# Optimization experiments

Measured on AMD Instinct MI355X. Metric: run time of the kernel, lower is better.

Reference implementation:

```python
import math
import jax, jax.numpy as jnp
import numpy as np


def setup_inputs() -> dict:
    key = jax.random.key(0)
    k1, k2 = jax.random.split(key)
    b, t, h, d = 2, 2048, 16, 64
    q = jax.random.normal(k1, (b, t, h, d), dtype=jnp.float32)
    kv = jax.random.normal(k2, (b, t, 2, h, d), dtype=jnp.float32)
    return {"q": q, "kv": kv}


def reference(q, kv):
    # Padded cross-attention branch, causal=False, dropout=0 (identity).
    d = q.shape[-1]
    softmax_scale = 1.0 / math.sqrt(d)
    k = kv[:, :, 0]  # [b, s, h, d]
    v = kv[:, :, 1]  # [b, s, h, d]
    # scores: [b, h, t, s] -- full score matrix, matching torch einsum
    scores = jnp.einsum('bthd,bshd->bhts', q, k * softmax_scale)
    attention = jax.nn.softmax(scores, axis=-1)
    out = jnp.einsum('bhts,bshd->bthd', attention, v)
    return out
```

## Files before the change

kernel.cpp:

```cpp
#include <hip/hip_runtime.h>
#include <hip/hip_bf16.h>

typedef __attribute__((ext_vector_type(8))) short v8s;
typedef __attribute__((ext_vector_type(4))) float v4f;
typedef unsigned long long u64;
typedef unsigned short u16;

#define BB 2
#define TT 2048
#define HH 16
#define DD 64


__device__ __forceinline__ unsigned short f2bf(float f) {
    unsigned int u = __builtin_bit_cast(unsigned int, f);
    u = u + 0x7FFFu + ((u >> 16) & 1u);
    return (unsigned short)(u >> 16);
}

__device__ __forceinline__ unsigned cvt2(float a, float b) {
    return ((unsigned)f2bf(b) << 16) | (unsigned)f2bf(a);
}

__device__ __forceinline__ v8s cvt8s(const float4& lo, const float4& hi, float s) {
    union { v8s v; unsigned u[4]; } r;
    r.u[0] = cvt2(lo.x * s, lo.y * s);
    r.u[1] = cvt2(lo.z * s, lo.w * s);
    r.u[2] = cvt2(hi.x * s, hi.y * s);
    r.u[3] = cvt2(hi.z * s, hi.w * s);
    return r.v;
}

__device__ __forceinline__ unsigned cvtpk(float lo, float hi) {
    unsigned r;
    asm("v_cvt_pk_bf16_f32 %0, %1, %2" : "=v"(r) : "v"(lo), "v"(hi));
    return r;
}

__device__ __forceinline__ v8s pack8(u64 lo, u64 hi) {
    union { v8s v; u64 q[2]; } u;
    u.q[0] = lo; u.q[1] = hi;
    return u.v;
}

typedef __attribute__((address_space(1))) const unsigned int gas_u32;
typedef __attribute__((address_space(3))) unsigned int las_u32;
__device__ __forceinline__ void gl_lds16(const void* g, void* l) {
    __builtin_amdgcn_global_load_lds((gas_u32*)g, (las_u32*)l, 16, 0, 0);
}


__global__ __launch_bounds__(256)
void prep_kv(const float* __restrict__ kvg, u16* __restrict__ wsK, u16* __restrict__ wsV) {
    __shared__ u16 vlds[64][72];
    const int wg   = blockIdx.x;
    const int tile = wg & 31;
    const int h    = (wg >> 5) & 15;
    const int b    = wg >> 9;
    const int t    = threadIdx.x;
    const int s0   = tile * 64;

    u16* kout = wsK + (((size_t)(b * 16 + h) * 32 + tile) * 4096);
    u16* vout = wsV + (((size_t)(b * 16 + h) * 32 + tile) * 4096);

    #pragma unroll
    for (int i = 0; i < 2; ++i) {
        int id  = t + 256 * i;
        int row = id >> 3;
        int bi  = id & 7;
        int c   = bi >> 2, lg = bi & 3;
        const float* kp = kvg + ((((size_t)(b * TT + s0 + row) * 2 + 0) * HH + h) * DD + 32 * c + 4 * lg);
        float4 ka = *(const float4*)kp;
        float4 kb = *(const float4*)(kp + 16);
        *(v8s*)((char*)kout + row * 128 + ((bi ^ (row & 7)) << 4)) = cvt8s(ka, kb, 1.0f);
    }
    #pragma unroll
    for (int i = 0; i < 2; ++i) {
        int id  = t + 256 * i;
        int row = id >> 3;
        int d8  = id & 7;
        const float* vp = kvg + ((((size_t)(b * TT + s0 + row) * 2 + 1) * HH + h) * DD + 8 * d8);
        float4 va = *(const float4*)vp;
        float4 vb = *(const float4*)(vp + 4);
        *(v8s*)&vlds[row][8 * d8] = cvt8s(va, vb, 1.0f);
    }
    __syncthreads();
    #pragma unroll
    for (int i = 0; i < 2; ++i) {
        int id = t + 256 * i;
        int dd = id >> 3;
        int bi = id & 7;
        int ks = bi >> 2, lg = bi & 3;
        union { v8s v; u16 w[8]; } r;
        #pragma unroll
        for (int j = 0; j < 4; ++j) {
            r.w[j]     = vlds[32 * ks + 4 * lg + j][dd];
            r.w[4 + j] = vlds[32 * ks + 16 + 4 * lg + j][dd];
        }
        *(v8s*)((char*)vout + dd * 128 + ((bi ^ (dd & 7)) << 4)) = r.v;
    }
}


__global__ __launch_bounds__(512, 4)
void attn_v4(const float* __restrict__ qg, const u16* __restrict__ wsK,
             const u16* __restrict__ wsV, float* __restrict__ outg) {
    __shared__ __align__(16) u16 KT[2][4096];
    __shared__ __align__(16) u16 VT[2][4096];

    const int bid  = blockIdx.x;
    const int wgid = (bid & 7) * 64 + (bid >> 3);
    const int qt   = wgid & 15;
    const int h    = (wgid >> 4) & 15;
    const int b    = wgid >> 8;
    const int tid  = threadIdx.x;
    const int lane = tid & 63;
    const int wid  = tid >> 6;
    const int lr   = lane & 15;
    const int lg   = lane >> 4;

    const u16* kbase = wsK + (size_t)(b * 16 + h) * 131072;
    const u16* vbase = wsV + (size_t)(b * 16 + h) * 131072;

    const int q0 = qt * 128 + wid * 16;

    const float qscale = 0.125f * 1.4426950408889634f;
    v8s qf[2];
    {
        const float* qb = qg + ((size_t)((b * TT + q0 + lr) * HH + h)) * DD;
        #pragma unroll
        for (int c = 0; c < 2; ++c) {
            float4 lo = *(const float4*)(qb + 32 * c + 4 * lg);
            float4 hi = *(const float4*)(qb + 32 * c + 4 * lg + 16);
            qf[c] = cvt8s(lo, hi, qscale);
        }
    }

#define STAGE(buf, tt)                                                                        \
    do {                                                                                      \
        gl_lds16(kbase + (size_t)(tt) * 4096 + tid * 8, (char*)&KT[buf][0] + wid * 1024);     \
        gl_lds16(vbase + (size_t)(tt) * 4096 + tid * 8, (char*)&VT[buf][0] + wid * 1024);     \
    } while (0)

    STAGE(0, 0);

    v4f oa[4];
    #pragma unroll
    for (int dc = 0; dc < 4; ++dc)
        #pragma unroll
        for (int r = 0; r < 4; ++r) oa[dc][r] = 0.0f;
    float m = -INFINITY, lsum = 0.0f;

    for (int t = 0; t < 32; ++t) {
        const int cur = t & 1;
        if (t < 31) {
            STAGE(cur ^ 1, t + 1);
            asm volatile("s_waitcnt vmcnt(2)" ::: "memory");
        } else {
            asm volatile("s_waitcnt vmcnt(0)" ::: "memory");
        }
        __builtin_amdgcn_s_barrier();

        const char* kb = (const char*)&KT[cur][0];
        const char* vb = (const char*)&VT[cur][0];

        v4f st[4];
        #pragma unroll
        for (int rb = 0; rb < 4; ++rb)
            #pragma unroll
            for (int r = 0; r < 4; ++r) st[rb][r] = 0.0f;
        __builtin_amdgcn_s_setprio(1);
        #pragma unroll
        for (int c = 0; c < 2; ++c) {
            #pragma unroll
            for (int rb = 0; rb < 4; ++rb) {
                int s = 16 * rb + lr;
                v8s kf = *(const v8s*)(kb + s * 128 + (((4 * c + lg) ^ (s & 7)) << 4));
                st[rb] = __builtin_amdgcn_mfma_f32_16x16x32_bf16(kf, qf[c], st[rb], 0, 0, 0);
            }
        }
        __builtin_amdgcn_s_setprio(0);

        float mc = st[0][0];
        #pragma unroll
        for (int rb = 0; rb < 4; ++rb)
            #pragma unroll
            for (int r = 0; r < 4; ++r) mc = fmaxf(mc, st[rb][r]);
        mc = fmaxf(mc, __shfl_xor(mc, 16));
        mc = fmaxf(mc, __shfl_xor(mc, 32));
        if (!__all(mc - m <= 8.0f)) {
            float mnew  = fmaxf(m, mc);
            float alpha = __builtin_amdgcn_exp2f(m - mnew);
            lsum *= alpha;
            m = mnew;
            float a0 = __shfl(alpha, 4 * lg + 0);
            float a1 = __shfl(alpha, 4 * lg + 1);
            float a2 = __shfl(alpha, 4 * lg + 2);
            float a3 = __shfl(alpha, 4 * lg + 3);
            #pragma unroll
            for (int dc = 0; dc < 4; ++dc) {
                oa[dc][0] *= a0; oa[dc][1] *= a1;
                oa[dc][2] *= a2; oa[dc][3] *= a3;
            }
        }
        float ps = 0.0f;
        #pragma unroll
        for (int rb = 0; rb < 4; ++rb)
            #pragma unroll
            for (int r = 0; r < 4; ++r) {
                float e = __builtin_amdgcn_exp2f(st[rb][r] - m);
                st[rb][r] = e;
                ps += e;
            }
        ps += __shfl_xor(ps, 16);
        ps += __shfl_xor(ps, 32);
        lsum += ps;

        v8s pf[2];
        #pragma unroll
        for (int ks = 0; ks < 2; ++ks) {
            union { v8s v; unsigned u[4]; } r;
            r.u[0] = cvtpk(st[2 * ks][0],     st[2 * ks][1]);
            r.u[1] = cvtpk(st[2 * ks][2],     st[2 * ks][3]);
            r.u[2] = cvtpk(st[2 * ks + 1][0], st[2 * ks + 1][1]);
            r.u[3] = cvtpk(st[2 * ks + 1][2], st[2 * ks + 1][3]);
            pf[ks] = r.v;
        }

        __builtin_amdgcn_s_setprio(1);
        #pragma unroll
        for (int ks = 0; ks < 2; ++ks) {
            #pragma unroll
            for (int dc = 0; dc < 4; ++dc) {
                int d = 16 * dc + lr;
                v8s vf = *(const v8s*)(vb + d * 128 + (((4 * ks + lg) ^ (d & 7)) << 4));
                oa[dc] = __builtin_amdgcn_mfma_f32_16x16x32_bf16(pf[ks], vf, oa[dc], 0, 0, 0);
            }
        }
        __builtin_amdgcn_s_setprio(0);

        __builtin_amdgcn_s_barrier();
    }

    float rl = 1.0f / lsum;
    float r0 = __shfl(rl, 4 * lg + 0);
    float r1 = __shfl(rl, 4 * lg + 1);
    float r2 = __shfl(rl, 4 * lg + 2);
    float r3 = __shfl(rl, 4 * lg + 3);
    #pragma unroll
    for (int dc = 0; dc < 4; ++dc) {
        size_t base = ((size_t)((b * TT + q0) * HH + h)) * DD + 16 * dc + lr;
        outg[base + (size_t)(4 * lg + 0) * HH * DD] = oa[dc][0] * r0;
        outg[base + (size_t)(4 * lg + 1) * HH * DD] = oa[dc][1] * r1;
        outg[base + (size_t)(4 * lg + 2) * HH * DD] = oa[dc][2] * r2;
        outg[base + (size_t)(4 * lg + 3) * HH * DD] = oa[dc][3] * r3;
    }
}


__global__ __launch_bounds__(256)
void attn_fwd_v1(const float* __restrict__ qg, const float* __restrict__ kvg,
                 float* __restrict__ outg) {
    __shared__ __align__(16) u16 Klds[32][68];
    __shared__ __align__(16) u16 Vt[DD][36];

    const int wg    = blockIdx.x;
    const int qtile = wg & 31;
    const int h     = (wg >> 5) & 15;
    const int b     = wg >> 9;
    const int tid   = threadIdx.x;
    const int lane  = tid & 63;
    const int wid   = tid >> 6;
    const int lr    = lane & 15;
    const int lg    = lane >> 4;
    const int q0    = qtile * 64 + wid * 16;

    const float qscale = 0.125f * 1.4426950408889634f;
    v8s qf[2];
    {
        const float* qb = qg + ((size_t)((b * TT + q0 + lr) * HH + h)) * DD;
        #pragma unroll
        for (int c = 0; c < 2; ++c) {
            float4 lo = *(const float4*)(qb + 32 * c + 4 * lg);
            float4 hi = *(const float4*)(qb + 32 * c + 4 * lg + 16);
            qf[c] = cvt8s(lo, hi, qscale);
        }
    }

    v4f oa[4];
    #pragma unroll
    for (int dc = 0; dc < 4; ++dc)
        #pragma unroll
        for (int r = 0; r < 4; ++r) oa[dc][r] = 0.0f;
    float m = -INFINITY, lsum = 0.0f;

    for (int kv0 = 0; kv0 < TT; kv0 += 32) {
        __syncthreads();
        #pragma unroll
        for (int i = 0; i < 2; ++i) {
            int id  = tid + 256 * i;
            int row = id >> 4;
            int cg  = (id & 15) * 4;
            const float* gp = kvg + ((size_t)(((b * TT + kv0 + row) * 2 + 0) * HH + h)) * DD + cg;
            float4 f = *(const float4*)gp;
            ushort4 w;
            w.x = f2bf(f.x); w.y = f2bf(f.y); w.z = f2bf(f.z); w.w = f2bf(f.w);
            *(ushort4*)&Klds[row][cg] = w;
        }
        {
            int s0 = tid >> 4;
            int dg = (tid & 15) * 4;
            const float* gp0 = kvg + ((size_t)(((b * TT + kv0 + 2 * s0) * 2 + 1) * HH + h)) * DD + dg;
            const float* gp1 = gp0 + 2 * HH * DD;
            float4 fa = *(const float4*)gp0;
            float4 fb = *(const float4*)gp1;
            float av[4] = {fa.x, fa.y, fa.z, fa.w};
            float bv[4] = {fb.x, fb.y, fb.z, fb.w};
            #pragma unroll
            for (int i = 0; i < 4; ++i) {
                ushort2 w;
                w.x = f2bf(av[i]);
                w.y = f2bf(bv[i]);
                *(ushort2*)&Vt[dg + i][2 * s0] = w;
            }
        }
        __syncthreads();

        v4f st0, st1;
        #pragma unroll
        for (int r = 0; r < 4; ++r) { st0[r] = 0.0f; st1[r] = 0.0f; }
        #pragma unroll
        for (int c = 0; c < 2; ++c) {
            {
                u64 lo = *(const u64*)&Klds[lr][32 * c + 4 * lg];
                u64 hi = *(const u64*)&Klds[lr][32 * c + 4 * lg + 16];
                st0 = __builtin_amdgcn_mfma_f32_16x16x32_bf16(pack8(lo, hi), qf[c], st0, 0, 0, 0);
            }
            {
                u64 lo = *(const u64*)&Klds[16 + lr][32 * c + 4 * lg];
                u64 hi = *(const u64*)&Klds[16 + lr][32 * c + 4 * lg + 16];
                st1 = __builtin_amdgcn_mfma_f32_16x16x32_bf16(pack8(lo, hi), qf[c], st1, 0, 0, 0);
            }
        }

        float sc[8] = {st0[0], st0[1], st0[2], st0[3], st1[0], st1[1], st1[2], st1[3]};
        float mc = sc[0];
        #pragma unroll
        for (int i = 1; i < 8; ++i) mc = fmaxf(mc, sc[i]);
        mc = fmaxf(mc, __shfl_xor(mc, 16));
        mc = fmaxf(mc, __shfl_xor(mc, 32));
        float mnew  = fmaxf(m, mc);
        float alpha = __builtin_amdgcn_exp2f(m - mnew);
        float p[8], ps = 0.0f;
        #pragma unroll
        for (int i = 0; i < 8; ++i) { p[i] = __builtin_amdgcn_exp2f(sc[i] - mnew); ps += p[i]; }
        ps += __shfl_xor(ps, 16);
        ps += __shfl_xor(ps, 32);
        lsum = lsum * alpha + ps;
        m = mnew;

        float ar0 = __shfl(alpha, 4 * lg + 0);
        float ar1 = __shfl(alpha, 4 * lg + 1);
        float ar2 = __shfl(alpha, 4 * lg + 2);
        float ar3 = __shfl(alpha, 4 * lg + 3);
        #pragma unroll
        for (int dc = 0; dc < 4; ++dc) {
            oa[dc][0] *= ar0; oa[dc][1] *= ar1; oa[dc][2] *= ar2; oa[dc][3] *= ar3;
        }

        v8s pf;
        #pragma unroll
        for (int i = 0; i < 8; ++i) pf[i] = (short)f2bf(p[i]);

        #pragma unroll
        for (int dc = 0; dc < 4; ++dc) {
            u64 lo = *(const u64*)&Vt[16 * dc + lr][4 * lg];
            u64 hi = *(const u64*)&Vt[16 * dc + lr][4 * lg + 16];
            oa[dc] = __builtin_amdgcn_mfma_f32_16x16x32_bf16(pf, pack8(lo, hi), oa[dc], 0, 0, 0);
        }
    }

    float rl  = 1.0f / lsum;
    float rr0 = __shfl(rl, 4 * lg + 0);
    float rr1 = __shfl(rl, 4 * lg + 1);
    float rr2 = __shfl(rl, 4 * lg + 2);
    float rr3 = __shfl(rl, 4 * lg + 3);
    #pragma unroll
    for (int dc = 0; dc < 4; ++dc) {
        size_t base = ((size_t)((b * TT + q0) * HH + h)) * DD + 16 * dc + lr;
        outg[base + (size_t)(4 * lg + 0) * HH * DD] = oa[dc][0] * rr0;
        outg[base + (size_t)(4 * lg + 1) * HH * DD] = oa[dc][1] * rr1;
        outg[base + (size_t)(4 * lg + 2) * HH * DD] = oa[dc][2] * rr2;
        outg[base + (size_t)(4 * lg + 3) * HH * DD] = oa[dc][3] * rr3;
    }
}

extern "C" void kernel_launch(void* const* d_in, const int* in_sizes, int n_in,
                              void* d_out, int out_size, void* d_ws, size_t ws_size,
                              hipStream_t stream) {
    const float* q  = (const float*)d_in[0];
    const float* kv = (const float*)d_in[1];
    float* out      = (float*)d_out;
    if (ws_size >= (size_t)16777216) {
        u16* wsK = (u16*)d_ws;
        u16* wsV = wsK + 4194304;
        hipLaunchKernelGGL(prep_kv, dim3(BB * HH * 32), dim3(256), 0, stream, kv, wsK, wsV);
        hipLaunchKernelGGL(attn_v4, dim3(512), dim3(512), 0, stream, q, wsK, wsV, out);
    } else {
        hipLaunchKernelGGL(attn_fwd_v1, dim3(1024), dim3(256), 0, stream, q, kv, out);
    }
}
```

Before: 65.51 us.

## Switch attention kernel to 32x32x16 MFMA with 32-row waves and 256-thread blocks

Replaces the 16x16x32 bf16 MFMA tiles with 32x32x16 tiles, so each wave handles 32 query rows and blocks shrink from 8 waves to 4. The prep kernel changes its K/V workspace swizzle to match the new fragment layout, and staging issues four loads per thread instead of two. The intent is fewer MFMA instructions and LDS fragment reads per FLOP, and fewer cross-lane shuffles for the row max, row sum and rescale. In exchange each wave holds larger accumulators, which raises register pressure, and with 4 waves per block there are fewer waves per block to hide latency.

Result: no change. 65.03 us (-0.7%).

```diff
diff --git a/kernel.cpp b/kernel.cpp
--- a/kernel.cpp
+++ b/kernel.cpp
@@ -1,8 +1,9 @@
 #include <hip/hip_runtime.h>
 #include <hip/hip_bf16.h>
 
-typedef __attribute__((ext_vector_type(8))) short v8s;
-typedef __attribute__((ext_vector_type(4))) float v4f;
+typedef __attribute__((ext_vector_type(8)))  short v8s;
+typedef __attribute__((ext_vector_type(4)))  float v4f;
+typedef __attribute__((ext_vector_type(16))) float v16f;
 typedef unsigned long long u64;
 typedef unsigned short u16;
 
@@ -68,10 +69,10 @@
         int id  = t + 256 * i;
         int row = id >> 3;
         int bi  = id & 7;
-        int c   = bi >> 2, lg = bi & 3;
-        const float* kp = kvg + ((((size_t)(b * TT + s0 + row) * 2 + 0) * HH + h) * DD + 32 * c + 4 * lg);
+        int c   = bi >> 1, hh = bi & 1;
+        const float* kp = kvg + ((((size_t)(b * TT + s0 + row) * 2 + 0) * HH + h) * DD + 16 * c + 4 * hh);
         float4 ka = *(const float4*)kp;
-        float4 kb = *(const float4*)(kp + 16);
+        float4 kb = *(const float4*)(kp + 8);
         *(v8s*)((char*)kout + row * 128 + ((bi ^ (row & 7)) << 4)) = cvt8s(ka, kb, 1.0f);
     }
     #pragma unroll
@@ -90,20 +91,20 @@
         int id = t + 256 * i;
         int dd = id >> 3;
         int bi = id & 7;
-        int ks = bi >> 2, lg = bi & 3;
+        int cc = bi >> 1, hh = bi & 1;
         union { v8s v; u16 w[8]; } r;
         #pragma unroll
         for (int j = 0; j < 4; ++j) {
-            r.w[j]     = vlds[32 * ks + 4 * lg + j][dd];
-            r.w[4 + j] = vlds[32 * ks + 16 + 4 * lg + j][dd];
+            r.w[j]     = vlds[16 * cc + 4 * hh + j][dd];
+            r.w[4 + j] = vlds[16 * cc + 8 + 4 * hh + j][dd];
         }
         *(v8s*)((char*)vout + dd * 128 + ((bi ^ (dd & 7)) << 4)) = r.v;
     }
 }
 
 
-__global__ __launch_bounds__(512, 4)
-void attn_v4(const float* __restrict__ qg, const u16* __restrict__ wsK,
+__global__ __launch_bounds__(256, 2)
+void attn_v5(const float* __restrict__ qg, const u16* __restrict__ wsK,
              const u16* __restrict__ wsV, float* __restrict__ outg) {
     __shared__ __align__(16) u16 KT[2][4096];
     __shared__ __align__(16) u16 VT[2][4096];
@@ -111,51 +112,54 @@
     const int bid  = blockIdx.x;
     const int wgid = (bid & 7) * 64 + (bid >> 3);
     const int qt   = wgid & 15;
-    const int h    = (wgid >> 4) & 15;
+    const int hH   = (wgid >> 4) & 15;
     const int b    = wgid >> 8;
     const int tid  = threadIdx.x;
     const int lane = tid & 63;
     const int wid  = tid >> 6;
-    const int lr   = lane & 15;
-    const int lg   = lane >> 4;
-
-    const u16* kbase = wsK + (size_t)(b * 16 + h) * 131072;
-    const u16* vbase = wsV + (size_t)(b * 16 + h) * 131072;
-
-    const int q0 = qt * 128 + wid * 16;
+    const int al   = lane & 31;
+    const int hh   = lane >> 5;
+
+    const u16* kbase = wsK + (size_t)(b * 16 + hH) * 131072;
+    const u16* vbase = wsV + (size_t)(b * 16 + hH) * 131072;
+
+    const int q0 = qt * 128 + wid * 32;
+    const int qr = q0 + al;
 
     const float qscale = 0.125f * 1.4426950408889634f;
-    v8s qf[2];
+    v8s qf[4];
     {
-        const float* qb = qg + ((size_t)((b * TT + q0 + lr) * HH + h)) * DD;
-        #pragma unroll
-        for (int c = 0; c < 2; ++c) {
-            float4 lo = *(const float4*)(qb + 32 * c + 4 * lg);
-            float4 hi = *(const float4*)(qb + 32 * c + 4 * lg + 16);
+        const float* qb = qg + ((size_t)((b * TT + qr) * HH + hH)) * DD;
+        #pragma unroll
+        for (int c = 0; c < 4; ++c) {
+            float4 lo = *(const float4*)(qb + 16 * c + 4 * hh);
+            float4 hi = *(const float4*)(qb + 16 * c + 4 * hh + 8);
             qf[c] = cvt8s(lo, hi, qscale);
         }
     }
 
-#define STAGE(buf, tt)                                                                        \
-    do {                                                                                      \
-        gl_lds16(kbase + (size_t)(tt) * 4096 + tid * 8, (char*)&KT[buf][0] + wid * 1024);     \
-        gl_lds16(vbase + (size_t)(tt) * 4096 + tid * 8, (char*)&VT[buf][0] + wid * 1024);     \
+#define STAGE(buf, tt)                                                                                    \
+    do {                                                                                                  \
+        gl_lds16(kbase + (size_t)(tt) * 4096 + tid * 8,        (char*)&KT[buf][0] + wid * 1024);          \
+        gl_lds16(kbase + (size_t)(tt) * 4096 + 2048 + tid * 8, (char*)&KT[buf][0] + 4096 + wid * 1024);   \
+        gl_lds16(vbase + (size_t)(tt) * 4096 + tid * 8,        (char*)&VT[buf][0] + wid * 1024);          \
+        gl_lds16(vbase + (size_t)(tt) * 4096 + 2048 + tid * 8, (char*)&VT[buf][0] + 4096 + wid * 1024);   \
     } while (0)
 
     STAGE(0, 0);
 
-    v4f oa[4];
-    #pragma unroll
-    for (int dc = 0; dc < 4; ++dc)
-        #pragma unroll
-        for (int r = 0; r < 4; ++r) oa[dc][r] = 0.0f;
+    v16f oa[2];
+    #pragma unroll
+    for (int dt = 0; dt < 2; ++dt)
+        #pragma unroll
+        for (int r = 0; r < 16; ++r) oa[dt][r] = 0.0f;
     float m = -INFINITY, lsum = 0.0f;
 
     for (int t = 0; t < 32; ++t) {
         const int cur = t & 1;
         if (t < 31) {
             STAGE(cur ^ 1, t + 1);
-            asm volatile("s_waitcnt vmcnt(2)" ::: "memory");
+            asm volatile("s_waitcnt vmcnt(4)" ::: "memory");
         } else {
             asm volatile("s_waitcnt vmcnt(0)" ::: "memory");
         }
@@ -164,77 +168,70 @@
         const char* kb = (const char*)&KT[cur][0];
         const char* vb = (const char*)&VT[cur][0];
 
-        v4f st[4];
-        #pragma unroll
-        for (int rb = 0; rb < 4; ++rb)
-            #pragma unroll
-            for (int r = 0; r < 4; ++r) st[rb][r] = 0.0f;
+        v16f st[2];
+        #pragma unroll
+        for (int kt = 0; kt < 2; ++kt)
+            #pragma unroll
+            for (int r = 0; r < 16; ++r) st[kt][r] = 0.0f;
         __builtin_amdgcn_s_setprio(1);
         #pragma unroll
-        for (int c = 0; c < 2; ++c) {
-            #pragma unroll
-            for (int rb = 0; rb < 4; ++rb) {
-                int s = 16 * rb + lr;
-                v8s kf = *(const v8s*)(kb + s * 128 + (((4 * c + lg) ^ (s & 7)) << 4));
-                st[rb] = __builtin_amdgcn_mfma_f32_16x16x32_bf16(kf, qf[c], st[rb], 0, 0, 0);
+        for (int c = 0; c < 4; ++c) {
+            #pragma unroll
+            for (int kt = 0; kt < 2; ++kt) {
+                int row = 32 * kt + al;
+                v8s kf = *(const v8s*)(kb + row * 128 + (((2 * c + hh) ^ (row & 7)) << 4));
+                st[kt] = __builtin_amdgcn_mfma_f32_32x32x16_bf16(kf, qf[c], st[kt], 0, 0, 0);
             }
         }
         __builtin_amdgcn_s_setprio(0);
 
         float mc = st[0][0];
         #pragma unroll
-        for (int rb = 0; rb < 4; ++rb)
-            #pragma unroll
-            for (int r = 0; r < 4; ++r) mc = fmaxf(mc, st[rb][r]);
-        mc = fmaxf(mc, __shfl_xor(mc, 16));
+        for (int kt = 0; kt < 2; ++kt)
+            #pragma unroll
+            for (int r = 0; r < 16; ++r) mc = fmaxf(mc, st[kt][r]);
         mc = fmaxf(mc, __shfl_xor(mc, 32));
         if (!__all(mc - m <= 8.0f)) {
             float mnew  = fmaxf(m, mc);
             float alpha = __builtin_amdgcn_exp2f(m - mnew);
             lsum *= alpha;
             m = mnew;
-            float a0 = __shfl(alpha, 4 * lg + 0);
-            float a1 = __shfl(alpha, 4 * lg + 1);
-            float a2 = __shfl(alpha, 4 * lg + 2);
-            float a3 = __shfl(alpha, 4 * lg + 3);
-            #pragma unroll
-            for (int dc = 0; dc < 4; ++dc) {
-                oa[dc][0] *= a0; oa[dc][1] *= a1;
-                oa[dc][2] *= a2; oa[dc][3] *= a3;
-            }
+            #pragma unroll
+            for (int dt = 0; dt < 2; ++dt)
+                #pragma unroll
+                for (int r = 0; r < 16; ++r) oa[dt][r] *= alpha;
         }
         float ps = 0.0f;
         #pragma unroll
-        for (int rb = 0; rb < 4; ++rb)
-            #pragma unroll
-            for (int r = 0; r < 4; ++r) {
-                float e = __builtin_amdgcn_exp2f(st[rb][r] - m);
-                st[rb][r] = e;
+        for (int kt = 0; kt < 2; ++kt)
+            #pragma unroll
+            for (int r = 0; r < 16; ++r) {
+                float e = __builtin_amdgcn_exp2f(st[kt][r] - m);
+                st[kt][r] = e;
                 ps += e;
             }
-        ps += __shfl_xor(ps, 16);
         ps += __shfl_xor(ps, 32);
         lsum += ps;
 
-        v8s pf[2];
-        #pragma unroll
-        for (int ks = 0; ks < 2; ++ks) {
+        v8s pf[4];
+        #pragma unroll
+        for (int cc = 0; cc < 4; ++cc) {
+            const int kt = cc >> 1, u8 = 8 * (cc & 1);
             union { v8s v; unsigned u[4]; } r;
-            r.u[0] = cvtpk(st[2 * ks][0],     st[2 * ks][1]);
-            r.u[1] = cvtpk(st[2 * ks][2],     st[2 * ks][3]);
-            r.u[2] = cvtpk(st[2 * ks + 1][0], st[2 * ks + 1][1]);
-            r.u[3] = cvtpk(st[2 * ks + 1][2], st[2 * ks + 1][3]);
-            pf[ks] = r.v;
+            #pragma unroll
+            for (int w = 0; w < 4; ++w)
+                r.u[w] = cvtpk(st[kt][u8 + 2 * w], st[kt][u8 + 2 * w + 1]);
+            pf[cc] = r.v;
         }
 
         __builtin_amdgcn_s_setprio(1);
         #pragma unroll
-        for (int ks = 0; ks < 2; ++ks) {
-            #pragma unroll
-            for (int dc = 0; dc < 4; ++dc) {
-                int d = 16 * dc + lr;
-                v8s vf = *(const v8s*)(vb + d * 128 + (((4 * ks + lg) ^ (d & 7)) << 4));
-                oa[dc] = __builtin_amdgcn_mfma_f32_16x16x32_bf16(pf[ks], vf, oa[dc], 0, 0, 0);
+        for (int cc = 0; cc < 4; ++cc) {
+            #pragma unroll
+            for (int dt = 0; dt < 2; ++dt) {
+                int row = 32 * dt + al;
+                v8s vf = *(const v8s*)(vb + row * 128 + (((2 * cc + hh) ^ (row & 7)) << 4));
+                oa[dt] = __builtin_amdgcn_mfma_f32_32x32x16_bf16(vf, pf[cc], oa[dt], 0, 0, 0);
             }
         }
         __builtin_amdgcn_s_setprio(0);
@@ -243,18 +240,14 @@
     }
 
     float rl = 1.0f / lsum;
-    float r0 = __shfl(rl, 4 * lg + 0);
-    float r1 = __shfl(rl, 4 * lg + 1);
-    float r2 = __shfl(rl, 4 * lg + 2);
-    float r3 = __shfl(rl, 4 * lg + 3);
-    #pragma unroll
-    for (int dc = 0; dc < 4; ++dc) {
-        size_t base = ((size_t)((b * TT + q0) * HH + h)) * DD + 16 * dc + lr;
-        outg[base + (size_t)(4 * lg + 0) * HH * DD] = oa[dc][0] * r0;
-        outg[base + (size_t)(4 * lg + 1) * HH * DD] = oa[dc][1] * r1;
-        outg[base + (size_t)(4 * lg + 2) * HH * DD] = oa[dc][2] * r2;
-        outg[base + (size_t)(4 * lg + 3) * HH * DD] = oa[dc][3] * r3;
-    }
+    const size_t obase = ((size_t)((b * TT + qr) * HH + hH)) * DD;
+    #pragma unroll
+    for (int dt = 0; dt < 2; ++dt)
+        #pragma unroll
+        for (int r = 0; r < 16; ++r) {
+            int d = 32 * dt + (r & 3) + 8 * (r >> 2) + 4 * hh;
+            outg[obase + d] = oa[dt][r] * rl;
+        }
 }
 
 
@@ -405,7 +398,7 @@
         u16* wsK = (u16*)d_ws;
         u16* wsV = wsK + 4194304;
         hipLaunchKernelGGL(prep_kv, dim3(BB * HH * 32), dim3(256), 0, stream, kv, wsK, wsV);
-        hipLaunchKernelGGL(attn_v4, dim3(512), dim3(512), 0, stream, q, wsK, wsV, out);
+        hipLaunchKernelGGL(attn_v5, dim3(512), dim3(256), 0, stream, q, wsK, wsV, out);
     } else {
         hipLaunchKernelGGL(attn_fwd_v1, dim3(1024), dim3(256), 0, stream, q, kv, out);
     }
```
